# Kernel optimization log

Measured on AMD Instinct MI355X. Metric: run time of the kernel, lower is better.

The kernel has to match this reference:

```python
import jax, jax.numpy as jnp
import numpy as np

B = 128          # graphs per batch
NP = 1024        # nodes per graph
FIN = 128        # input node features
H = 128          # hidden width (SAGEConv out)
C = 10           # output classes
N = B * NP
DEG = 16
E = N * DEG
K1 = int(np.ceil(0.8 * NP))   # 820
K2 = int(np.ceil(0.8 * K1))   # 656
K3 = int(np.ceil(0.8 * K2))   # 525


def setup_inputs() -> dict:
    key = jax.random.key(0)
    k = jax.random.split(key, 16)
    x = jax.random.normal(k[0], (N, FIN), jnp.float32)
    # edges constrained within each graph (PyG batched-graph semantics)
    g = jnp.arange(E, dtype=jnp.int32) // (E // B)
    src = g * NP + jax.random.randint(k[1], (E,), 0, NP, jnp.int32)
    dst = g * NP + jax.random.randint(k[2], (E,), 0, NP, jnp.int32)
    edge_index = jnp.stack([src, dst])

    def lin(kk, o, i):
        return jax.random.normal(kk, (o, i), jnp.float32) / np.sqrt(i)

    return {
        'x': x, 'edge_index': edge_index,
        'Wl1': lin(k[3], H, FIN), 'bl1': jnp.zeros((H,), jnp.float32), 'Wr1': lin(k[4], H, FIN),
        'wp1': jax.random.normal(k[5], (H,), jnp.float32),
        'Wl2': lin(k[6], H, H), 'bl2': jnp.zeros((H,), jnp.float32), 'Wr2': lin(k[7], H, H),
        'wp2': jax.random.normal(k[8], (H,), jnp.float32),
        'Wl3': lin(k[9], H, H), 'bl3': jnp.zeros((H,), jnp.float32), 'Wr3': lin(k[10], H, H),
        'wp3': jax.random.normal(k[11], (H,), jnp.float32),
        'Wf1': lin(k[12], 64, H), 'bf1': jnp.zeros((64,), jnp.float32),
        'Wf2': lin(k[13], C, 64), 'bf2': jnp.zeros((C,), jnp.float32),
    }


def _sage(x, src, dst, em, Wl, bl, Wr):
    # PyG SAGEConv: lin_l(mean_{j in N(i)} x_j) + lin_r(x_i); edge mask em kills pruned edges
    msg = x[src] * em[:, None]                                   # [E,H] gather
    s = jax.ops.segment_sum(msg, dst, num_segments=N)            # scatter-add
    deg = jax.ops.segment_sum(em, dst, num_segments=N)
    mean = s / jnp.maximum(deg, 1.0)[:, None]
    return mean @ Wl.T + bl + x @ Wr.T


def _topk(x, w, nm, kk):
    # TopKPooling: score = x.w/||w||, keep top ceil(ratio*n) per graph, gate kept nodes by tanh(score)
    score = (x @ w) / (jnp.linalg.norm(w) + 1e-16)               # [N]
    s2 = jnp.where(nm, score, -jnp.inf).reshape(B, NP)
    _, idx = jax.lax.top_k(s2, kk)                               # [B,kk] static shape
    sel = jnp.zeros((B, NP), bool).at[jnp.arange(B)[:, None], idx].set(True).reshape(-1)
    x = jnp.where(sel[:, None], x * jnp.tanh(score)[:, None], 0.0)
    return x, sel


def _forward(x, Wl1, bl1, Wr1, wp1, Wl2, bl2, Wr2, wp2, Wl3, bl3, Wr3, wp3,
             Wf1, bf1, Wf2, bf2, edge_index):
    src, dst = edge_index[0], edge_index[1]
    nm = jnp.ones((N,), bool)                 # node alive mask
    em = jnp.ones((E,), jnp.float32)          # edge alive mask
    for (Wl, bl, Wr, wp, kk) in ((Wl1, bl1, Wr1, wp1, K1),
                                 (Wl2, bl2, Wr2, wp2, K2),
                                 (Wl3, bl3, Wr3, wp3, K3)):
        x = jax.nn.relu(_sage(x, src, dst, em, Wl, bl, Wr))
        x, nm = _topk(x, wp, nm, kk)
        em = (nm[src] & nm[dst]).astype(jnp.float32)
    # global_mean_pool over surviving nodes per graph (pruned nodes are exactly zero)
    cnt = nm.reshape(B, NP).sum(1).astype(x.dtype)
    pooled = x.reshape(B, NP, H).sum(1) / jnp.maximum(cnt, 1.0)[:, None]
    h = jax.nn.relu(pooled @ Wf1.T + bf1)
    return jax.nn.log_softmax(h @ Wf2.T + bf2, axis=-1)


def reference(x, edge_index, Wl1, bl1, Wr1, wp1, Wl2, bl2, Wr2, wp2,
              Wl3, bl3, Wr3, wp3, Wf1, bf1, Wf2, bf2):
    return _forward(x, Wl1, bl1, Wr1, wp1, Wl2, bl2, Wr2, wp2,
                    Wl3, bl3, Wr3, wp3, Wf1, bf1, Wf2, bf2, edge_index)
```

## Files before the change

### kernel.cpp

```cpp
#include <hip/hip_runtime.h>

constexpr int NGPH = 128;
constexpr int NPG  = 1024;
constexpr int NN   = NGPH * NPG;
constexpr int HD   = 128;
constexpr int EPG  = 16384;
constexpr int KS1 = 820, KS2 = 656, KS3 = 525;

typedef _Float16 half4v __attribute__((ext_vector_type(4)));
typedef _Float16 half8v __attribute__((ext_vector_type(8)));
typedef float f32x4 __attribute__((ext_vector_type(4)));

__global__ __launch_bounds__(256) void init_gate(float* __restrict__ gate) {
  int i = blockIdx.x * 256 + threadIdx.x;
  if (i < NN) gate[i] = 1.0f;
}

__global__ __launch_bounds__(512) void csr_build(int* __restrict__ ei) {
  __shared__ unsigned int ed[EPG];
  __shared__ int cnt[NPG];
  __shared__ int scn[NPG];
  __shared__ int off[NPG];
  int g = blockIdx.x, t = threadIdx.x;
  const int* srcg = ei + (size_t)g * EPG;
  const int* dstg = ei + (size_t)NGPH * EPG + (size_t)g * EPG;
  for (int i = t; i < EPG; i += 512) {
    unsigned int s = (unsigned int)(srcg[i] - (g << 10));
    unsigned int d = (unsigned int)(dstg[i] - (g << 10));
    ed[i] = s | (d << 10);
  }
  for (int i = t; i < NPG; i += 512) cnt[i] = 0;
  __syncthreads();
  for (int i = t; i < EPG; i += 512) atomicAdd(&cnt[ed[i] >> 10], 1);
  __syncthreads();
  int* a = cnt; int* b = scn;
  for (int d = 1; d < NPG; d <<= 1) {
    for (int i = t; i < NPG; i += 512) b[i] = a[i] + (i >= d ? a[i - d] : 0);
    __syncthreads();
    int* tmp = a; a = b; b = tmp;
  }
  unsigned short* ssort = (unsigned short*)(ei + (size_t)g * EPG);
  unsigned short* rsout = ssort + EPG;
  for (int r = t; r < NPG; r += 512) {
    int ex = r ? a[r - 1] : 0;
    rsout[r] = (unsigned short)ex;
    off[r] = ex;
  }
  __syncthreads();
  for (int i = t; i < EPG; i += 512) {
    unsigned int e = ed[i];
    int pos = atomicAdd(&off[e >> 10], 1);
    ssort[pos] = (unsigned short)(e & 1023u);
  }
}

__global__ __launch_bounds__(256) void wsplit(const float* __restrict__ Wl,
                                              const float* __restrict__ Wr,
                                              _Float16* __restrict__ WH) {
  int i = blockIdx.x * 256 + threadIdx.x;
  int n = i >> 8, k = i & 255;
  float v = (k < 128) ? Wl[n * HD + k] : Wr[n * HD + (k - 128)];
  _Float16 h = (_Float16)v;
  WH[i] = h;
  WH[32768 + i] = (_Float16)(v - (float)h);
}

__global__ __launch_bounds__(256) void agg2_kernel(const float* __restrict__ X,
                                                   const int* __restrict__ ei,
                                                   const float* __restrict__ gate,
                                                   float* __restrict__ Mout) {
  int t = threadIdx.x;
  int xcd = blockIdx.x & 7, q = blockIdx.x >> 3;
  int g = ((q >> 7) << 3) + xcd;
  int r = (q & 127) * 8 + (t >> 5);
  int lane = t & 31;
  int gbase = g << 10;

  if (gate[gbase + r] == 0.f) return;

  const unsigned short* ss  = (const unsigned short*)(ei + (size_t)g * EPG);
  const unsigned short* rsg = ss + EPG;
  int start = rsg[r];
  int end   = (r < 1023) ? (int)rsg[r + 1] : EPG;
  const float4* X4 = (const float4*)X;
  size_t gb4 = (size_t)gbase * 32;
  float4 acc = make_float4(0.f, 0.f, 0.f, 0.f);
  float degf = 0.f;
  for (int base = start; base < end; base += 32) {
    int ec = end - base; if (ec > 32) ec = 32;
    int sl = 0; float gv = 0.f;
    if (lane < ec) {
      sl = ss[base + lane];
      gv = gate[gbase + sl];
    }
    degf += (gv != 0.f) ? 1.f : 0.f;
    int e = 0;
    for (; e + 4 <= ec; e += 4) {
      int s0 = __shfl(sl, e, 32),     s1 = __shfl(sl, e + 1, 32);
      int s2 = __shfl(sl, e + 2, 32), s3 = __shfl(sl, e + 3, 32);
      float g0 = __shfl(gv, e, 32),     g1 = __shfl(gv, e + 1, 32);
      float g2 = __shfl(gv, e + 2, 32), g3 = __shfl(gv, e + 3, 32);
      float4 v0 = X4[gb4 + (size_t)s0 * 32 + lane];
      float4 v1 = X4[gb4 + (size_t)s1 * 32 + lane];
      float4 v2 = X4[gb4 + (size_t)s2 * 32 + lane];
      float4 v3 = X4[gb4 + (size_t)s3 * 32 + lane];
      acc.x += v0.x * g0 + v1.x * g1 + v2.x * g2 + v3.x * g3;
      acc.y += v0.y * g0 + v1.y * g1 + v2.y * g2 + v3.y * g3;
      acc.z += v0.z * g0 + v1.z * g1 + v2.z * g2 + v3.z * g3;
      acc.w += v0.w * g0 + v1.w * g1 + v2.w * g2 + v3.w * g3;
    }
    for (; e < ec; ++e) {
      int s0 = __shfl(sl, e, 32);
      float g0 = __shfl(gv, e, 32);
      float4 v0 = X4[gb4 + (size_t)s0 * 32 + lane];
      acc.x += v0.x * g0; acc.y += v0.y * g0;
      acc.z += v0.z * g0; acc.w += v0.w * g0;
    }
  }
#pragma unroll
  for (int m = 1; m <= 16; m <<= 1) degf += __shfl_xor(degf, m, 32);
  float inv = 1.0f / fmaxf(degf, 1.0f);
  acc.x *= inv; acc.y *= inv; acc.z *= inv; acc.w *= inv;
  ((float4*)Mout)[(size_t)(gbase + r) * 32 + lane] = acc;
}

constexpr int LDA = 40;
__global__ __launch_bounds__(256) void gemm_mfma(const float* S,
                                                 const float* __restrict__ X,
                                                 const _Float16* __restrict__ WH,
                                                 const float* __restrict__ bb,
                                                 const float* __restrict__ wp,
                                                 const float* __restrict__ gate,
                                                 float* Hout,
                                                 float* __restrict__ score) {
  __shared__ _Float16 Ah[128 * LDA];
  __shared__ _Float16 Al[128 * LDA];
  __shared__ float gsh[128];
  __shared__ float sc_s[128];
  int t = threadIdx.x;
  int r0 = blockIdx.x * 128;
  int lane = t & 63, wid = t >> 6;
  int wm = wid & 1, wn = wid >> 1;
  int quad = lane >> 4, mr = lane & 15;

  if (t < 128) { gsh[t] = gate[r0 + t]; sc_s[t] = 0.f; }
  __syncthreads();

  f32x4 acc[4][4];
#pragma unroll
  for (int i = 0; i < 4; ++i)
#pragma unroll
    for (int j = 0; j < 4; ++j) acc[i][j] = (f32x4){0.f, 0.f, 0.f, 0.f};

  for (int ks = 0; ks < 256; ks += 32) {
    bool isS = (ks < 128);
    const float* Asrc = isS ? (S + (size_t)r0 * HD + ks)
                            : (X + (size_t)r0 * HD + (ks - 128));
#pragma unroll
    for (int i = 0; i < 4; ++i) {
      int f = t + i * 256;
      int row = f >> 3;
      int kq = (f & 7) * 4;
      float4 v = *(const float4*)&Asrc[(size_t)row * HD + kq];
      if (!isS) {
        float gv = gsh[row];
        v.x *= gv; v.y *= gv; v.z *= gv; v.w *= gv;
      }
      half4v h, l;
      h.x = (_Float16)v.x; h.y = (_Float16)v.y; h.z = (_Float16)v.z; h.w = (_Float16)v.w;
      l.x = (_Float16)(v.x - (float)h.x); l.y = (_Float16)(v.y - (float)h.y);
      l.z = (_Float16)(v.z - (float)h.z); l.w = (_Float16)(v.w - (float)h.w);
      *(half4v*)&Ah[row * LDA + kq] = h;
      *(half4v*)&Al[row * LDA + kq] = l;
    }
    __syncthreads();
    half8v af[4], alf[4], bf[4], blf[4];
#pragma unroll
    for (int i = 0; i < 4; ++i) {
      int rowA = (wm * 64 + i * 16 + mr) * LDA + quad * 8;
      af[i]  = *(const half8v*)&Ah[rowA];
      alf[i] = *(const half8v*)&Al[rowA];
    }
#pragma unroll
    for (int j = 0; j < 4; ++j) {
      const _Float16* bp = WH + (wn * 64 + j * 16 + mr) * 256 + ks + quad * 8;
      bf[j]  = *(const half8v*)bp;
      blf[j] = *(const half8v*)(bp + 32768);
    }
#pragma unroll
    for (int i = 0; i < 4; ++i)
#pragma unroll
      for (int j = 0; j < 4; ++j) {
        acc[i][j] = __builtin_amdgcn_mfma_f32_16x16x32_f16(af[i],  bf[j],  acc[i][j], 0, 0, 0);
        acc[i][j] = __builtin_amdgcn_mfma_f32_16x16x32_f16(af[i],  blf[j], acc[i][j], 0, 0, 0);
        acc[i][j] = __builtin_amdgcn_mfma_f32_16x16x32_f16(alf[i], bf[j],  acc[i][j], 0, 0, 0);
      }
    __syncthreads();
  }
  float p[4][4];
#pragma unroll
  for (int i = 0; i < 4; ++i)
#pragma unroll
    for (int r = 0; r < 4; ++r) p[i][r] = 0.f;
#pragma unroll
  for (int j = 0; j < 4; ++j) {
    int col = wn * 64 + j * 16 + mr;
    float bias = bb[col];
    float wv = wp[col];
#pragma unroll
    for (int i = 0; i < 4; ++i) {
      int rowl = wm * 64 + i * 16 + quad * 4;
#pragma unroll
      for (int r = 0; r < 4; ++r) {
        bool alive = (gsh[rowl + r] != 0.f);
        float ho = alive ? fmaxf(acc[i][j][r] + bias, 0.f) : 0.f;
        Hout[(size_t)(r0 + rowl + r) * HD + col] = ho;
        p[i][r] += ho * wv;
      }
    }
  }
#pragma unroll
  for (int i = 0; i < 4; ++i)
#pragma unroll
    for (int r = 0; r < 4; ++r) {
#pragma unroll
      for (int m = 1; m <= 8; m <<= 1) p[i][r] += __shfl_xor(p[i][r], m, 16);
      if (mr == 0) atomicAdd(&sc_s[wm * 64 + i * 16 + quad * 4 + r], p[i][r]);
    }
  __syncthreads();
  if (t < 128) score[r0 + t] = sc_s[t];
}

__global__ __launch_bounds__(256) void topk_kernel(const float* __restrict__ score,
                                                   float* __restrict__ gate,
                                                   const float* __restrict__ wp,
                                                   int kk) {
  __shared__ float sc[NPG];
  __shared__ unsigned key[NPG];
  __shared__ int hist[256];
  __shared__ float shv;
  __shared__ unsigned s_pfx;
  __shared__ int s_need;
  int g = blockIdx.x, t = threadIdx.x;
  int gb = g << 10;
  if (t == 0) {
    float ss = 0.f;
    for (int i = 0; i < HD; ++i) ss += wp[i] * wp[i];
    shv = 1.0f / (sqrtf(ss) + 1e-16f);
    s_pfx = 0u; s_need = kk;
  }
  __syncthreads();
  float inv = shv;
#pragma unroll
  for (int q = 0; q < 4; ++q) {
    int n = t + q * 256;
    float s = score[gb + n] * inv;
    sc[n] = s;
    unsigned u = __float_as_uint(s);
    u = (u & 0x80000000u) ? ~u : (u | 0x80000000u);
    key[n] = (gate[gb + n] != 0.f) ? u : 0u;
  }
  for (int shift = 24; shift >= 0; shift -= 8) {
    hist[t] = 0;
    __syncthreads();
    unsigned pfx = s_pfx;
    unsigned mask = (shift == 24) ? 0u : (0xFFFFFFFFu << (shift + 8));
#pragma unroll
    for (int q = 0; q < 4; ++q) {
      unsigned u = key[t + q * 256];
      if ((u & mask) == (pfx & mask))
        atomicAdd(&hist[(u >> shift) & 255], 1);
    }
    __syncthreads();
    if (t < 64) {
      int c0 = hist[t * 4 + 0], c1 = hist[t * 4 + 1];
      int c2 = hist[t * 4 + 2], c3 = hist[t * 4 + 3];
      int s3 = c3, s2 = c2 + s3, s1 = c1 + s2, s0 = c0 + s1;
      int tot = s0;
      int suf = tot;
#pragma unroll
      for (int off = 1; off < 64; off <<= 1) {
        int v = __shfl_down(suf, off, 64);
        if (t + off < 64) suf += v;
      }
      int above = suf - tot;
      int need = s_need;
      int best = -1;
      if      (above + s3 >= need) best = t * 4 + 3;
      else if (above + s2 >= need) best = t * 4 + 2;
      else if (above + s1 >= need) best = t * 4 + 1;
      else if (above + s0 >= need) best = t * 4 + 0;
#pragma unroll
      for (int off = 1; off < 64; off <<= 1) {
        int v = __shfl_xor(best, off, 64);
        best = best > v ? best : v;
      }
      if ((best >> 2) == t) {
        int j = best & 3;
        int sj = (j == 0) ? s0 : (j == 1) ? s1 : (j == 2) ? s2 : s3;
        int cj = (j == 0) ? c0 : (j == 1) ? c1 : (j == 2) ? c2 : c3;
        s_need = need - (above + sj - cj);
        s_pfx  = pfx | ((unsigned)best << shift);
      }
    }
    __syncthreads();
  }
  unsigned thr = s_pfx;
#pragma unroll
  for (int q = 0; q < 4; ++q) {
    int n = t + q * 256;
    bool sel = (key[n] != 0u) && (key[n] >= thr);
    gate[gb + n] = sel ? tanhf(sc[n]) : 0.f;
  }
}

__global__ __launch_bounds__(512) void final_kernel(const float* __restrict__ X,
                                                    const float* __restrict__ gate,
                                                    const float* __restrict__ Wf1,
                                                    const float* __restrict__ bf1,
                                                    const float* __restrict__ Wf2,
                                                    const float* __restrict__ bf2,
                                                    float* __restrict__ out) {
  __shared__ float gs[NPG];
  __shared__ float4 part[16][32];
  __shared__ float pl[HD];
  __shared__ float h1[64];
  __shared__ float lg[10];
  __shared__ float red[2];
  int g = blockIdx.x, t = threadIdx.x;
  for (int i = t; i < NPG; i += 512) gs[i] = gate[(g << 10) + i];
  __syncthreads();
  int slot = t & 31, chunk = t >> 5;
  const float4* X4 = (const float4*)X + (size_t)(g << 10) * 32;
  float4 acc = make_float4(0.f, 0.f, 0.f, 0.f);
  for (int rr = 0; rr < 64; ++rr) {
    int row = chunk * 64 + rr;
    float w = gs[row];
    if (w != 0.f) {
      float4 v = X4[(size_t)row * 32 + slot];
      acc.x += v.x * w; acc.y += v.y * w; acc.z += v.z * w; acc.w += v.w * w;
    }
  }
  part[chunk][slot] = acc;
  __syncthreads();
  if (t < 32) {
    float4 s = part[0][t];
#pragma unroll
    for (int c = 1; c < 16; ++c) {
      float4 p = part[c][t];
      s.x += p.x; s.y += p.y; s.z += p.z; s.w += p.w;
    }
    float k = 1.0f / (float)KS3;
    pl[t * 4 + 0] = s.x * k; pl[t * 4 + 1] = s.y * k;
    pl[t * 4 + 2] = s.z * k; pl[t * 4 + 3] = s.w * k;
  }
  __syncthreads();
  if (t < 64) {
    float h = bf1[t];
    for (int f = 0; f < HD; ++f) h += pl[f] * Wf1[t * HD + f];
    h1[t] = fmaxf(h, 0.f);
  }
  __syncthreads();
  if (t < 10) {
    float z = bf2[t];
    for (int j = 0; j < 64; ++j) z += h1[j] * Wf2[t * 64 + j];
    lg[t] = z;
  }
  __syncthreads();
  if (t == 0) {
    float m = lg[0];
    for (int c = 1; c < 10; ++c) m = fmaxf(m, lg[c]);
    float ssum = 0.f;
    for (int c = 0; c < 10; ++c) ssum += expf(lg[c] - m);
    red[0] = m; red[1] = logf(ssum);
  }
  __syncthreads();
  if (t < 10) out[g * 10 + t] = lg[t] - red[0] - red[1];
}

extern "C" void kernel_launch(void* const* d_in, const int* in_sizes, int n_in,
                              void* d_out, int out_size, void* d_ws, size_t ws_size,
                              hipStream_t stream) {
  const float* x  = (const float*)d_in[0];
  int* ei         = (int*)d_in[1];
  const float* Wl[3]  = {(const float*)d_in[2], (const float*)d_in[6],  (const float*)d_in[10]};
  const float* blv[3] = {(const float*)d_in[3], (const float*)d_in[7],  (const float*)d_in[11]};
  const float* Wr[3]  = {(const float*)d_in[4], (const float*)d_in[8],  (const float*)d_in[12]};
  const float* wp[3]  = {(const float*)d_in[5], (const float*)d_in[9],  (const float*)d_in[13]};
  const float* Wf1 = (const float*)d_in[14];
  const float* bf1 = (const float*)d_in[15];
  const float* Wf2 = (const float*)d_in[16];
  const float* bf2 = (const float*)d_in[17];
  float* out = (float*)d_out;

  float* bufA  = (float*)d_ws;
  float* bufB  = bufA + (size_t)NN * HD;
  float* gate  = bufB + (size_t)NN * HD;
  float* score = gate + NN;

  _Float16* wpl = (_Float16*)(ei + (size_t)NGPH * EPG);

  init_gate<<<NN / 256, 256, 0, stream>>>(gate);
  csr_build<<<NGPH, 512, 0, stream>>>(ei);
  wsplit<<<128, 256, 0, stream>>>(Wl[0], Wr[0], wpl);
  wsplit<<<128, 256, 0, stream>>>(Wl[1], Wr[1], wpl + 65536);
  wsplit<<<128, 256, 0, stream>>>(Wl[2], Wr[2], wpl + 131072);

  agg2_kernel<<<NN / 8, 256, 0, stream>>>(x, ei, gate, bufA);
  gemm_mfma<<<NN / 128, 256, 0, stream>>>(bufA, x, wpl, blv[0], wp[0], gate, bufA, score);
  topk_kernel<<<NGPH, 256, 0, stream>>>(score, gate, wp[0], KS1);
  agg2_kernel<<<NN / 8, 256, 0, stream>>>(bufA, ei, gate, bufB);
  gemm_mfma<<<NN / 128, 256, 0, stream>>>(bufB, bufA, wpl + 65536, blv[1], wp[1], gate, bufB, score);
  topk_kernel<<<NGPH, 256, 0, stream>>>(score, gate, wp[1], KS2);
  agg2_kernel<<<NN / 8, 256, 0, stream>>>(bufB, ei, gate, bufA);
  gemm_mfma<<<NN / 128, 256, 0, stream>>>(bufA, bufB, wpl + 131072, blv[2], wp[2], gate, bufA, score);
  topk_kernel<<<NGPH, 256, 0, stream>>>(score, gate, wp[2], KS3);

  final_kernel<<<NGPH, 512, 0, stream>>>(bufA, gate, Wf1, bf1, Wf2, bf2, out);
}
```

Before: 541.6 us.

## Emit pre-split fp16 hi/lo aggregates and software-prefetch GEMM A tiles

The aggregation kernel now writes the mean-aggregated features directly as fp16 hi/lo pairs instead of fp32, so the GEMM no longer has to convert the S half itself. The GEMM gains register-level prefetching: the next K-slice of the pre-split S and of X is loaded into registers while the current slice is in LDS and being consumed by MFMA. This is meant to hide global-load latency and cut conversion work. The cost is higher register pressure and more complex control flow. The written byte count for S stays the same, since hi and lo together take as much space as one fp32 value.

```diff
diff --git a/kernel.cpp b/kernel.cpp
--- a/kernel.cpp
+++ b/kernel.cpp
@@ -68,7 +68,7 @@
 __global__ __launch_bounds__(256) void agg2_kernel(const float* __restrict__ X,
                                                    const int* __restrict__ ei,
                                                    const float* __restrict__ gate,
-                                                   float* __restrict__ Mout) {
+                                                   _Float16* __restrict__ Sp) {
   int t = threadIdx.x;
   int xcd = blockIdx.x & 7, q = blockIdx.x >> 3;
   int g = ((q >> 7) << 3) + xcd;
@@ -121,11 +121,18 @@
   for (int m = 1; m <= 16; m <<= 1) degf += __shfl_xor(degf, m, 32);
   float inv = 1.0f / fmaxf(degf, 1.0f);
   acc.x *= inv; acc.y *= inv; acc.z *= inv; acc.w *= inv;
-  ((float4*)Mout)[(size_t)(gbase + r) * 32 + lane] = acc;
+  half4v h, l;
+  h.x = (_Float16)acc.x; h.y = (_Float16)acc.y;
+  h.z = (_Float16)acc.z; h.w = (_Float16)acc.w;
+  l.x = (_Float16)(acc.x - (float)h.x); l.y = (_Float16)(acc.y - (float)h.y);
+  l.z = (_Float16)(acc.z - (float)h.z); l.w = (_Float16)(acc.w - (float)h.w);
+  size_t rowb = (size_t)(gbase + r) * 256;
+  *(half4v*)&Sp[rowb + lane * 4]       = h;
+  *(half4v*)&Sp[rowb + 128 + lane * 4] = l;
 }
 
 constexpr int LDA = 40;
-__global__ __launch_bounds__(256) void gemm_mfma(const float* S,
+__global__ __launch_bounds__(256) void gemm_mfma(const _Float16* Sp,
                                                  const float* __restrict__ X,
                                                  const _Float16* __restrict__ WH,
                                                  const float* __restrict__ bb,
@@ -143,6 +150,17 @@
   int wm = wid & 1, wn = wid >> 1;
   int quad = lane >> 4, mr = lane & 15;
 
+  int c0 = t, c1 = t + 256;
+  int row0 = c0 >> 2, kq0 = (c0 & 3) * 8;
+  int row1 = c1 >> 2, kq1 = (c1 & 3) * 8;
+  const char* spb = (const char*)(Sp + (size_t)r0 * 256);
+
+  int4 ph0 = *(const int4*)(spb + row0 * 512 + kq0 * 2);
+  int4 ph1 = *(const int4*)(spb + row1 * 512 + kq1 * 2);
+  int4 pl0 = *(const int4*)(spb + row0 * 512 + 256 + kq0 * 2);
+  int4 pl1 = *(const int4*)(spb + row1 * 512 + 256 + kq1 * 2);
+  float4 px[4];
+
   if (t < 128) { gsh[t] = gate[r0 + t]; sc_s[t] = 0.f; }
   __syncthreads();
 
@@ -152,20 +170,62 @@
 #pragma unroll
     for (int j = 0; j < 4; ++j) acc[i][j] = (f32x4){0.f, 0.f, 0.f, 0.f};
 
-  for (int ks = 0; ks < 256; ks += 32) {
-    bool isS = (ks < 128);
-    const float* Asrc = isS ? (S + (size_t)r0 * HD + ks)
-                            : (X + (size_t)r0 * HD + (ks - 128));
+  half8v af[4], alf[4], bf[4], blf[4];
+
+  for (int ks = 0; ks < 128; ks += 32) {
+    *(int4*)&Ah[row0 * LDA + kq0] = ph0;
+    *(int4*)&Ah[row1 * LDA + kq1] = ph1;
+    *(int4*)&Al[row0 * LDA + kq0] = pl0;
+    *(int4*)&Al[row1 * LDA + kq1] = pl1;
+    if (ks < 96) {
+      int ko = (ks + 32) * 2;
+      ph0 = *(const int4*)(spb + row0 * 512 + ko + kq0 * 2);
+      ph1 = *(const int4*)(spb + row1 * 512 + ko + kq1 * 2);
+      pl0 = *(const int4*)(spb + row0 * 512 + 256 + ko + kq0 * 2);
+      pl1 = *(const int4*)(spb + row1 * 512 + 256 + ko + kq1 * 2);
+    } else {
+      const float* Asrc = X + (size_t)r0 * HD;
+#pragma unroll
+      for (int i = 0; i < 4; ++i) {
+        int f = t + i * 256;
+        int row = f >> 3;
+        int kq = (f & 7) * 4;
+        px[i] = *(const float4*)&Asrc[(size_t)row * HD + kq];
+      }
+    }
+    __syncthreads();
+#pragma unroll
+    for (int i = 0; i < 4; ++i) {
+      int rowA = (wm * 64 + i * 16 + mr) * LDA + quad * 8;
+      af[i]  = *(const half8v*)&Ah[rowA];
+      alf[i] = *(const half8v*)&Al[rowA];
+    }
+#pragma unroll
+    for (int j = 0; j < 4; ++j) {
+      const _Float16* bp = WH + (wn * 64 + j * 16 + mr) * 256 + ks + quad * 8;
+      bf[j]  = *(const half8v*)bp;
+      blf[j] = *(const half8v*)(bp + 32768);
+    }
+#pragma unroll
+    for (int i = 0; i < 4; ++i)
+#pragma unroll
+      for (int j = 0; j < 4; ++j) {
+        acc[i][j] = __builtin_amdgcn_mfma_f32_16x16x32_f16(af[i],  bf[j],  acc[i][j], 0, 0, 0);
+        acc[i][j] = __builtin_amdgcn_mfma_f32_16x16x32_f16(af[i],  blf[j], acc[i][j], 0, 0, 0);
+        acc[i][j] = __builtin_amdgcn_mfma_f32_16x16x32_f16(alf[i], bf[j],  acc[i][j], 0, 0, 0);
+      }
+    __syncthreads();
+  }
+
+  for (int ks = 128; ks < 256; ks += 32) {
 #pragma unroll
     for (int i = 0; i < 4; ++i) {
       int f = t + i * 256;
       int row = f >> 3;
       int kq = (f & 7) * 4;
-      float4 v = *(const float4*)&Asrc[(size_t)row * HD + kq];
-      if (!isS) {
-        float gv = gsh[row];
-        v.x *= gv; v.y *= gv; v.z *= gv; v.w *= gv;
-      }
+      float gv = gsh[row];
+      float4 v = px[i];
+      v.x *= gv; v.y *= gv; v.z *= gv; v.w *= gv;
       half4v h, l;
       h.x = (_Float16)v.x; h.y = (_Float16)v.y; h.z = (_Float16)v.z; h.w = (_Float16)v.w;
       l.x = (_Float16)(v.x - (float)h.x); l.y = (_Float16)(v.y - (float)h.y);
@@ -173,8 +233,17 @@
       *(half4v*)&Ah[row * LDA + kq] = h;
       *(half4v*)&Al[row * LDA + kq] = l;
     }
-    __syncthreads();
-    half8v af[4], alf[4], bf[4], blf[4];
+    if (ks < 224) {
+      const float* Asrc = X + (size_t)r0 * HD + (ks - 96);
+#pragma unroll
+      for (int i = 0; i < 4; ++i) {
+        int f = t + i * 256;
+        int row = f >> 3;
+        int kq = (f & 7) * 4;
+        px[i] = *(const float4*)&Asrc[(size_t)row * HD + kq];
+      }
+    }
+    __syncthreads();
 #pragma unroll
     for (int i = 0; i < 4; ++i) {
       int rowA = (wm * 64 + i * 16 + mr) * LDA + quad * 8;
@@ -197,6 +266,7 @@
       }
     __syncthreads();
   }
+
   float p[4][4];
 #pragma unroll
   for (int i = 0; i < 4; ++i)
@@ -397,6 +467,8 @@
   float* bufB  = bufA + (size_t)NN * HD;
   float* gate  = bufB + (size_t)NN * HD;
   float* score = gate + NN;
+  _Float16* spA = (_Float16*)bufA;
+  _Float16* spB = (_Float16*)bufB;
 
   _Float16* wpl = (_Float16*)(ei + (size_t)NGPH * EPG);
 
@@ -406,14 +478,14 @@
   wsplit<<<128, 256, 0, stream>>>(Wl[1], Wr[1], wpl + 65536);
   wsplit<<<128, 256, 0, stream>>>(Wl[2], Wr[2], wpl + 131072);
 
-  agg2_kernel<<<NN / 8, 256, 0, stream>>>(x, ei, gate, bufA);
-  gemm_mfma<<<NN / 128, 256, 0, stream>>>(bufA, x, wpl, blv[0], wp[0], gate, bufA, score);
+  agg2_kernel<<<NN / 8, 256, 0, stream>>>(x, ei, gate, spA);
+  gemm_mfma<<<NN / 128, 256, 0, stream>>>(spA, x, wpl, blv[0], wp[0], gate, bufA, score);
   topk_kernel<<<NGPH, 256, 0, stream>>>(score, gate, wp[0], KS1);
-  agg2_kernel<<<NN / 8, 256, 0, stream>>>(bufA, ei, gate, bufB);
-  gemm_mfma<<<NN / 128, 256, 0, stream>>>(bufB, bufA, wpl + 65536, blv[1], wp[1], gate, bufB, score);
+  agg2_kernel<<<NN / 8, 256, 0, stream>>>(bufA, ei, gate, spB);
+  gemm_mfma<<<NN / 128, 256, 0, stream>>>(spB, bufA, wpl + 65536, blv[1], wp[1], gate, bufB, score);
   topk_kernel<<<NGPH, 256, 0, stream>>>(score, gate, wp[1], KS2);
-  agg2_kernel<<<NN / 8, 256, 0, stream>>>(bufB, ei, gate, bufA);
-  gemm_mfma<<<NN / 128, 256, 0, stream>>>(bufA, bufB, wpl + 131072, blv[2], wp[2], gate, bufA, score);
+  agg2_kernel<<<NN / 8, 256, 0, stream>>>(bufB, ei, gate, spA);
+  gemm_mfma<<<NN / 128, 256, 0, stream>>>(spA, bufB, wpl + 131072, blv[2], wp[2], gate, bufA, score);
   topk_kernel<<<NGPH, 256, 0, stream>>>(score, gate, wp[2], KS3);
 
   final_kernel<<<NGPH, 512, 0, stream>>>(bufA, gate, Wf1, bf1, Wf2, bf2, out);
```

After: 508.2 us. 1.07x faster.
